# Kernel optimization log

Hardware: AMD Instinct MI355X
Metric: run time of the kernel (lower is better)

The kernel has to match this reference:

```python
import jax, jax.numpy as jnp
import numpy as np

NPOINT, RADIUS, NSAMPLE = 1024, 0.4, 32
BN_EPS = 1e-5


def fps(xyz, npoint):
    # xyz: [B, N, 3]. Deterministic start at index 0 (torch uses randint).
    B, N, _ = xyz.shape

    def step(carry, _):
        distance, farthest = carry  # [B,N], [B]
        centroid = jnp.take_along_axis(xyz, farthest[:, None, None], axis=1)  # [B,1,3]
        dist = jnp.sum((xyz - centroid) ** 2, -1)  # [B,N]
        distance = jnp.minimum(distance, dist)
        new_far = jnp.argmax(distance, axis=-1).astype(jnp.int32)
        return (distance, new_far), farthest

    init = (jnp.full((B, N), 1e10, xyz.dtype), jnp.zeros((B,), jnp.int32))
    _, cents = jax.lax.scan(step, init, None, length=npoint)  # [npoint, B]
    return cents.T  # [B, npoint]


def square_distance(src, dst):
    # src [B,S,3], dst [B,N,3] -> [B,S,N]
    d = -2.0 * jnp.einsum('bsc,bnc->bsn', src, dst)
    d = d + jnp.sum(src ** 2, -1)[:, :, None] + jnp.sum(dst ** 2, -1)[:, None, :]
    return jnp.clip(d, 1e-12, None)


def query_ball_point(radius, nsample, xyz, new_xyz):
    B, N, _ = xyz.shape
    S = new_xyz.shape[1]
    sqr = square_distance(new_xyz, xyz)  # [B,S,N]
    gi = jnp.where(sqr > radius ** 2, N, jnp.arange(N, dtype=jnp.int32)[None, None, :])
    gi = jnp.sort(gi, axis=-1)[:, :, :nsample]  # [B,S,K]
    first = gi[:, :, :1]
    return jnp.where(gi == N, first, gi)


def gather_points(points, idx):
    # points [B,N,C], idx [B,S,K] -> [B,S,K,C]
    B, S, K = idx.shape
    C = points.shape[-1]
    flat = jnp.take_along_axis(points, idx.reshape(B, S * K)[:, :, None], axis=1)
    return flat.reshape(B, S, K, C)


def setup_inputs() -> dict:
    key = jax.random.key(0)
    ks = jax.random.split(key, 10)
    B, N, D = 8, 4096, 64
    inp = {
        'xyz': jax.random.normal(ks[0], (B, 3, N), jnp.float32),
        'points': jax.random.normal(ks[1], (B, D, N), jnp.float32),
    }
    chans = [67, 64, 64, 128]
    for i in range(3):
        cin, cout = chans[i], chans[i + 1]
        inp[f'W{i}'] = jax.random.normal(ks[2 + i], (cout, cin), jnp.float32) * (1.0 / np.sqrt(cin))
        inp[f'b{i}'] = jnp.zeros((cout,), jnp.float32)
        inp[f'g{i}'] = jnp.ones((cout,), jnp.float32)
        inp[f'bt{i}'] = jnp.zeros((cout,), jnp.float32)
    return inp


def _forward(xyz, points, Ws, bs, gs, bts):
    xyz_t = jnp.transpose(xyz, (0, 2, 1))      # [B,N,3]
    pts_t = jnp.transpose(points, (0, 2, 1))   # [B,N,D]
    B, N, _ = xyz_t.shape

    fps_idx = fps(xyz_t, NPOINT)                              # [B,S]
    new_xyz = jnp.take_along_axis(xyz_t, fps_idx[:, :, None], axis=1)  # [B,S,3]
    idx = query_ball_point(RADIUS, NSAMPLE, xyz_t, new_xyz)   # [B,S,K]

    grouped_xyz = gather_points(xyz_t, idx)                   # [B,S,K,3]
    grouped_xyz_norm = grouped_xyz - new_xyz[:, :, None, :]
    grouped_pts = gather_points(pts_t, idx)                   # [B,S,K,D]
    new_points = jnp.concatenate([grouped_xyz_norm, grouped_pts], -1)  # [B,S,K,3+D]

    x = jnp.transpose(new_points, (0, 3, 2, 1))  # [B,C,K,S]
    for W, b, g, bt in zip(Ws, bs, gs, bts):
        x = jnp.einsum('oc,bcks->boks', W, x) + b[None, :, None, None]
        mean = jnp.mean(x, axis=(0, 2, 3), keepdims=True)
        var = jnp.var(x, axis=(0, 2, 3), keepdims=True)
        x = (x - mean) * jax.lax.rsqrt(var + BN_EPS)
        x = x * g[None, :, None, None] + bt[None, :, None, None]
        x = jax.nn.relu(x)
    out = jnp.max(x, axis=2)                      # [B,C_out,S]
    return jnp.transpose(new_xyz, (0, 2, 1)), out


def reference(xyz, points, W0, b0, g0, bt0, W1, b1, g1, bt1, W2, b2, g2, bt2):
    return _forward(xyz, points, (W0, W1, W2), (b0, b1, b2), (g0, g1, g2), (bt0, bt1, bt2))
```

## Files before the change

### kernel.cpp

```cpp
#include <hip/hip_runtime.h>
#include <cstddef>
#include <cstdint>

#define NB 8
#define NPTS 4096
#define NS 1024
#define NK 32
#define ND 64

#define DPP_IMAX(v, ctrl)                                                     \
  {                                                                           \
    int _o = __builtin_amdgcn_update_dpp(v, v, ctrl, 0xf, 0xf, false);        \
    v = (_o > v) ? _o : v;                                                    \
  }

#define DPP_U64MAX(hi, lo, ctrl)                                              \
  {                                                                           \
    unsigned _nh = (unsigned)__builtin_amdgcn_update_dpp((int)(hi), (int)(hi),\
                                                         ctrl, 0xf, 0xf, false);\
    unsigned _nl = (unsigned)__builtin_amdgcn_update_dpp((int)(lo), (int)(lo),\
                                                         ctrl, 0xf, 0xf, false);\
    bool _gt = (_nh > (hi)) || (_nh == (hi) && _nl > (lo));                   \
    hi = _gt ? _nh : (hi);                                                    \
    lo = _gt ? _nl : (lo);                                                    \
  }

#define DPP_FADD(v, ctrl)                                                     \
  {                                                                           \
    int _t = __builtin_amdgcn_update_dpp(__float_as_int(v), __float_as_int(v),\
                                         ctrl, 0xf, 0xf, false);              \
    v = v + __int_as_float(_t);                                               \
  }

__global__ __launch_bounds__(512) void fps_pgemm_kernel(
    const float* __restrict__ xyz, float* __restrict__ out_newxyz,
    float* __restrict__ ws_newxyz, const float* __restrict__ points,
    const float* __restrict__ W0, const float* __restrict__ b0g,
    float* __restrict__ P1) {
  __shared__ __align__(16) char smem[53376];
  const int t = threadIdx.x;

  if (blockIdx.x < 8) {
    float* sXYZ = (float*)smem;
    unsigned long long(*sRed)[8] =
        (unsigned long long(*)[8])(smem + 49152);
    int* sWidx = (int*)(smem + 49280);
    const int b = blockIdx.x;
    const int wave = t >> 6;
    const int lane = t & 63;
    const float* xb = xyz + (size_t)b * 3 * NPTS;

    for (int i = t; i < NPTS; i += 512) {
      sXYZ[i * 3 + 0] = xb[i];
      sXYZ[i * 3 + 1] = xb[NPTS + i];
      sXYZ[i * 3 + 2] = xb[2 * NPTS + i];
    }
    if (t == 0) sWidx[0] = 0;

    float px[8], py[8], pz[8], dist[8];
    {
      float4 a0 = ((const float4*)xb)[2 * t];
      float4 a1 = ((const float4*)xb)[2 * t + 1];
      float4 b0v = ((const float4*)(xb + NPTS))[2 * t];
      float4 b1v = ((const float4*)(xb + NPTS))[2 * t + 1];
      float4 c0 = ((const float4*)(xb + 2 * NPTS))[2 * t];
      float4 c1 = ((const float4*)(xb + 2 * NPTS))[2 * t + 1];
      px[0] = a0.x; px[1] = a0.y; px[2] = a0.z; px[3] = a0.w;
      px[4] = a1.x; px[5] = a1.y; px[6] = a1.z; px[7] = a1.w;
      py[0] = b0v.x; py[1] = b0v.y; py[2] = b0v.z; py[3] = b0v.w;
      py[4] = b1v.x; py[5] = b1v.y; py[6] = b1v.z; py[7] = b1v.w;
      pz[0] = c0.x; pz[1] = c0.y; pz[2] = c0.z; pz[3] = c0.w;
      pz[4] = c1.x; pz[5] = c1.y; pz[6] = c1.z; pz[7] = c1.w;
    }
#pragma unroll
    for (int j = 0; j < 8; ++j) dist[j] = 1e10f;

    float cx = xb[0], cy = xb[NPTS], cz = xb[2 * NPTS];

    for (int s = 0; s < NS; ++s) {
#pragma unroll
      for (int j = 0; j < 8; ++j) {
        float dx = __fadd_rn(px[j], -cx);
        float dy = __fadd_rn(py[j], -cy);
        float dz = __fadd_rn(pz[j], -cz);
        float d = __fadd_rn(__fadd_rn(__fmul_rn(dx, dx), __fmul_rn(dy, dy)),
                            __fmul_rn(dz, dz));
        dist[j] = fminf(dist[j], d);
      }
      float m = fmaxf(fmaxf(fmaxf(dist[0], dist[1]), fmaxf(dist[2], dist[3])),
                      fmaxf(fmaxf(dist[4], dist[5]), fmaxf(dist[6], dist[7])));
      int v = __float_as_int(m);
      DPP_IMAX(v, 0x111)
      DPP_IMAX(v, 0x112)
      DPP_IMAX(v, 0x114)
      DPP_IMAX(v, 0x118)
      DPP_IMAX(v, 0x142)
      DPP_IMAX(v, 0x143)
      const int wm_i = __builtin_amdgcn_readlane(v, 63);
      const float wm = __int_as_float(wm_i);
      unsigned long long claim = __ballot(m == wm);
      int firstlane = __ffsll(claim) - 1;
      if (lane == firstlane) {
        int j = 7;
#pragma unroll
        for (int jj = 6; jj >= 0; --jj)
          if (dist[jj] == wm) j = jj;
        unsigned widx = (unsigned)(t * 8 + j);
        sRed[s & 1][wave] = ((unsigned long long)(unsigned)wm_i << 32) |
                            (unsigned long long)(0xFFFFFFFFu - widx);
      }
      __syncthreads();
      unsigned long long k = sRed[s & 1][lane & 7];
      unsigned h2 = (unsigned)(k >> 32), l2 = (unsigned)k;
      DPP_U64MAX(h2, l2, 0x111)
      DPP_U64MAX(h2, l2, 0x112)
      DPP_U64MAX(h2, l2, 0x114)
      const unsigned gl = (unsigned)__builtin_amdgcn_readlane((int)l2, 7);
      const int widx = (int)(0xFFFFFFFFu - gl);
      cx = sXYZ[widx * 3 + 0];
      cy = sXYZ[widx * 3 + 1];
      cz = sXYZ[widx * 3 + 2];
      if (t == 0 && s < NS - 1) sWidx[s + 1] = widx;
    }
    __syncthreads();
    for (int s2 = t; s2 < NS; s2 += 512) {
      int w = sWidx[s2];
      float x = sXYZ[w * 3 + 0], y = sXYZ[w * 3 + 1], z = sXYZ[w * 3 + 2];
      out_newxyz[b * 3 * NS + s2] = x;
      out_newxyz[b * 3 * NS + NS + s2] = y;
      out_newxyz[b * 3 * NS + 2 * NS + s2] = z;
      ws_newxyz[((b << 10) + s2) * 3 + 0] = x;
      ws_newxyz[((b << 10) + s2) * 3 + 1] = y;
      ws_newxyz[((b << 10) + s2) * 3 + 2] = z;
    }
  } else {
    float* sP = (float*)smem;
    float* sW = (float*)(smem + 16384);
    float* sB = (float*)(smem + 33792);
    const int blk = blockIdx.x - 8;
    const int bb = blk >> 6;
    const int n0 = (blk & 63) * 64;
    const float* pb = points + (size_t)bb * ND * NPTS;
    for (int f = t; f < 4096; f += 512) {
      int c = f >> 6, n = f & 63;
      sP[f] = pb[c * NPTS + n0 + n];
    }
    for (int f = t; f < 4096; f += 512) {
      int c = f >> 6, o = f & 63;
      sW[c * 68 + o] = W0[o * 67 + 3 + c];
    }
    if (t < 64) sB[t] = b0g[t];
    __syncthreads();
    if (t < 256) {
      const int nl = (t & 15) * 4;
      const int ol = (t >> 4) * 4;
      float acc[4][4];
#pragma unroll
      for (int i = 0; i < 4; ++i)
#pragma unroll
        for (int j = 0; j < 4; ++j) acc[i][j] = 0.f;
#pragma unroll 4
      for (int c = 0; c < 64; ++c) {
        float4 xv = *(const float4*)(sP + c * 64 + nl);
        float4 wv = *(const float4*)(sW + c * 68 + ol);
        float xa[4] = {xv.x, xv.y, xv.z, xv.w};
        float wa[4] = {wv.x, wv.y, wv.z, wv.w};
#pragma unroll
        for (int i = 0; i < 4; ++i)
#pragma unroll
          for (int j = 0; j < 4; ++j) acc[i][j] += xa[i] * wa[j];
      }
#pragma unroll
      for (int i = 0; i < 4; ++i) {
        float4 v = make_float4(acc[i][0] + sB[ol + 0], acc[i][1] + sB[ol + 1],
                               acc[i][2] + sB[ol + 2], acc[i][3] + sB[ol + 3]);
        *(float4*)(P1 + ((size_t)(bb << 12) + n0 + nl + i) * 64 + ol) = v;
      }
    }
  }
}

__global__ __launch_bounds__(256) void query_gstats_kernel(
    const float* __restrict__ xyz, const float* __restrict__ ws_newxyz,
    const float* __restrict__ P1, const float* __restrict__ W0,
    int* __restrict__ idx_ws, float* __restrict__ partials) {
  const int w = threadIdx.x >> 6;
  const int lane = threadIdx.x & 63;
  const int p = blockIdx.x * 4 + w;
  const int b = p >> 10;
  __shared__ int sIdx[4][32];
  __shared__ float sWS[4][64];
  __shared__ float sWQ[4][64];
  const float* xb = xyz + (size_t)b * 3 * NPTS;
  const float cx = ws_newxyz[p * 3 + 0];
  const float cy = ws_newxyz[p * 3 + 1];
  const float cz = ws_newxyz[p * 3 + 2];
  const float ss = __fadd_rn(__fadd_rn(__fmul_rn(cx, cx), __fmul_rn(cy, cy)), __fmul_rn(cz, cz));
  const float r2 = (float)(0.4 * 0.4);
  int cnt = 0;
  for (int ci = 0; ci < 64 && cnt < 32; ++ci) {
    int n = ci * 64 + lane;
    float x = xb[n], y = xb[NPTS + n], z = xb[2 * NPTS + n];
    float dot = __fadd_rn(__fadd_rn(__fmul_rn(cx, x), __fmul_rn(cy, y)), __fmul_rn(cz, z));
    float dd = __fadd_rn(__fadd_rn(__fmul_rn(x, x), __fmul_rn(y, y)), __fmul_rn(z, z));
    float d = __fmul_rn(-2.0f, dot);
    d = __fadd_rn(d, ss);
    d = __fadd_rn(d, dd);
    d = fmaxf(d, 1e-12f);
    bool inc = (d <= r2);
    unsigned long long m = __ballot(inc);
    int slot = cnt + (int)__popcll(m & ((1ull << lane) - 1ull));
    if (inc && slot < 32) sIdx[w][slot] = n;
    cnt += (int)__popcll(m);
  }
  if (lane < 32) {
    int v;
    if (lane < cnt) v = sIdx[w][lane];
    else v = (cnt > 0) ? sIdx[w][0] : 0;
    idx_ws[p * 32 + lane] = v;
    sIdx[w][lane] = v;
  }
  const float wx = W0[lane * 67 + 0];
  const float wy = W0[lane * 67 + 1];
  const float wz = W0[lane * 67 + 2];
  float ssum = 0.f, ssq = 0.f;
  for (int r = 0; r < 32; ++r) {
    const int n = sIdx[w][r];
    float P1v = P1[((size_t)(b << 12) + n) * 64 + lane];
    float dx = __fadd_rn(xb[n], -cx);
    float dy = __fadd_rn(xb[NPTS + n], -cy);
    float dz = __fadd_rn(xb[2 * NPTS + n], -cz);
    float y = P1v + (dx * wx + dy * wy + dz * wz);
    ssum += y;
    ssq += y * y;
  }
  sWS[w][lane] = ssum;
  sWQ[w][lane] = ssq;
  __syncthreads();
  const int t = threadIdx.x;
  if (t < 64) {
    float s1 = sWS[0][t] + sWS[1][t] + sWS[2][t] + sWS[3][t];
    float s2 = sWQ[0][t] + sWQ[1][t] + sWQ[2][t] + sWQ[3][t];
    partials[(size_t)blockIdx.x * 128 + t] = s1;
    partials[(size_t)blockIdx.x * 128 + 64 + t] = s2;
  }
}

__global__ __launch_bounds__(256) void conv1_kernel(
    const float* __restrict__ xyz, const float* __restrict__ P1,
    const int* __restrict__ idx_ws, const float* __restrict__ cen_ws,
    const float* __restrict__ W0, const float* __restrict__ W1,
    const float* __restrict__ bias, const float* __restrict__ scaleA,
    const float* __restrict__ shiftA, float* __restrict__ y1,
    float* __restrict__ partials) {
  constexpr int CIN = 64, COUT = 64, WP = 68, TPS = 128;
  __shared__ __align__(16) float sW[CIN * WP];
  __shared__ __align__(16) float sX[2 * CIN * 32];
  __shared__ float sY[64 * 65];
  __shared__ int sIdx[64];
  __shared__ float sCen[2 * 4];
  __shared__ float sScale[CIN];
  __shared__ float sShift[CIN];
  __shared__ float sSum[COUT];
  __shared__ float sSq[COUT];

  const int t = threadIdx.x;
  const int wave = t >> 6, lane = t & 63;
  const int pair0 = blockIdx.x * 2;
  const int b = pair0 >> 10;

  for (int f = t; f < CIN * COUT; f += 256) {
    int o = f / CIN;
    int c = f - o * CIN;
    sW[c * WP + o] = W1[f];
  }
  if (t < CIN) { sScale[t] = scaleA[t]; sShift[t] = shiftA[t]; }
  if (t < COUT) { sSum[t] = 0.f; sSq[t] = 0.f; }
  if (t < 64) sIdx[t] = idx_ws[pair0 * 32 + t];
  if (t < 6) sCen[(t / 3) * 4 + (t % 3)] = cen_ws[pair0 * 3 + t];
  const float wx = W0[lane * 67 + 0];
  const float wy = W0[lane * 67 + 1];
  const float wz = W0[lane * 67 + 2];
  __syncthreads();
  const float* xb = xyz + (size_t)b * 3 * NPTS;
  for (int r = wave; r < 64; r += 4) {
    const int sl = r >> 5;
    const int n = sIdx[r];
    float P1v = P1[((size_t)(b << 12) + n) * 64 + lane];
    float dx = __fadd_rn(xb[n], -sCen[sl * 4 + 0]);
    float dy = __fadd_rn(xb[NPTS + n], -sCen[sl * 4 + 1]);
    float dz = __fadd_rn(xb[2 * NPTS + n], -sCen[sl * 4 + 2]);
    sY[r * 65 + lane] = P1v + (dx * wx + dy * wy + dz * wz);
  }
  __syncthreads();
  for (int f = t; f < 2 * CIN * 32; f += 256) {
    int sl = f >> 11;
    int rmd = f & 2047;
    int o = rmd >> 5, k = rmd & 31;
    float v = sY[(sl * 32 + k) * 65 + o];
    v = v * sScale[o] + sShift[o];
    sX[f] = fmaxf(v, 0.f);
  }
  __syncthreads();

  const int sl = t / TPS;
  const int tl = t - sl * TPS;
  const int k0 = (tl & 7) * 4;
  const int o0 = (tl >> 3) * 4;

  float acc[4][4];
#pragma unroll
  for (int i = 0; i < 4; ++i)
#pragma unroll
    for (int j = 0; j < 4; ++j) acc[i][j] = 0.f;

  const float* xrow = sX + sl * (CIN * 32);
#pragma unroll 4
  for (int c = 0; c < CIN; ++c) {
    float4 xv = *(const float4*)(xrow + c * 32 + k0);
    float4 wv = *(const float4*)(sW + c * WP + o0);
    float xa[4] = {xv.x, xv.y, xv.z, xv.w};
    float wa[4] = {wv.x, wv.y, wv.z, wv.w};
#pragma unroll
    for (int i = 0; i < 4; ++i)
#pragma unroll
      for (int j = 0; j < 4; ++j) acc[i][j] += wa[i] * xa[j];
  }
#pragma unroll
  for (int i = 0; i < 4; ++i) {
    float bo = bias[o0 + i];
#pragma unroll
    for (int j = 0; j < 4; ++j) acc[i][j] += bo;
  }
#pragma unroll
  for (int i = 0; i < 4; ++i) {
    float s1 = (acc[i][0] + acc[i][1]) + (acc[i][2] + acc[i][3]);
    float s2 = (acc[i][0] * acc[i][0] + acc[i][1] * acc[i][1]) +
               (acc[i][2] * acc[i][2] + acc[i][3] * acc[i][3]);
    DPP_FADD(s1, 0x111)
    DPP_FADD(s1, 0x112)
    DPP_FADD(s1, 0x114)
    DPP_FADD(s2, 0x111)
    DPP_FADD(s2, 0x112)
    DPP_FADD(s2, 0x114)
    if ((t & 7) == 7) {
      atomicAdd(&sSum[o0 + i], s1);
      atomicAdd(&sSq[o0 + i], s2);
    }
  }
#pragma unroll
  for (int i = 0; i < 4; ++i) {
    float4 v = make_float4(acc[i][0], acc[i][1], acc[i][2], acc[i][3]);
    *(float4*)(y1 + (size_t)(pair0 + sl) * COUT * 32 + (o0 + i) * 32 + k0) = v;
  }
  __syncthreads();
  if (t < COUT) {
    partials[(size_t)blockIdx.x * (COUT * 2) + t] = sSum[t];
    partials[(size_t)blockIdx.x * (COUT * 2) + COUT + t] = sSq[t];
  }
}

template <int CIN, int COUT, int SPB, int MODE>
__global__ __launch_bounds__(256) void conv_kernel(
    const float* __restrict__ xin, const float* __restrict__ W,
    const float* __restrict__ bias, const float* __restrict__ scaleA,
    const float* __restrict__ shiftA, float* __restrict__ yout,
    float* __restrict__ pmax, float* __restrict__ pmin,
    float* __restrict__ partials) {
  constexpr int WP = COUT + 4;
  constexpr int TPS = (COUT / 4) * 8;
  __shared__ __align__(16) float sW[CIN * WP];
  __shared__ __align__(16) float sX[SPB * CIN * 32];
  __shared__ float sScale[CIN];
  __shared__ float sShift[CIN];
  __shared__ float sSum[COUT];
  __shared__ float sSq[COUT];
  __shared__ float sMax[8 * COUT];
  __shared__ float sMin[8 * COUT];

  const int t = threadIdx.x;
  const int pair0 = blockIdx.x * SPB;

  for (int f = t; f < CIN * COUT; f += 256) {
    int o = f / CIN;
    int c = f - o * CIN;
    sW[c * WP + o] = W[f];
  }
  if (t < CIN) { sScale[t] = scaleA[t]; sShift[t] = shiftA[t]; }
  if (t < COUT) { sSum[t] = 0.f; sSq[t] = 0.f; }
  __syncthreads();

  for (int f = t; f < SPB * CIN * 32; f += 256) {
    int c = (f >> 5) % CIN;
    float v = xin[(size_t)pair0 * CIN * 32 + f];
    v = v * sScale[c] + sShift[c];
    sX[f] = fmaxf(v, 0.f);
  }
  __syncthreads();

  const int sl = t / TPS;
  const int tl = t - sl * TPS;
  const int k0 = (tl & 7) * 4;
  const int o0 = (tl >> 3) * 4;

  float acc[4][4];
#pragma unroll
  for (int i = 0; i < 4; ++i)
#pragma unroll
    for (int j = 0; j < 4; ++j) acc[i][j] = 0.f;

  const float* xrow = sX + sl * (CIN * 32);
#pragma unroll 4
  for (int c = 0; c < CIN; ++c) {
    float4 xv = *(const float4*)(xrow + c * 32 + k0);
    float4 wv = *(const float4*)(sW + c * WP + o0);
    float xa[4] = {xv.x, xv.y, xv.z, xv.w};
    float wa[4] = {wv.x, wv.y, wv.z, wv.w};
#pragma unroll
    for (int i = 0; i < 4; ++i)
#pragma unroll
      for (int j = 0; j < 4; ++j) acc[i][j] += wa[i] * xa[j];
  }
#pragma unroll
  for (int i = 0; i < 4; ++i) {
    float bo = bias[o0 + i];
#pragma unroll
    for (int j = 0; j < 4; ++j) acc[i][j] += bo;
  }
#pragma unroll
  for (int i = 0; i < 4; ++i) {
    float s1 = (acc[i][0] + acc[i][1]) + (acc[i][2] + acc[i][3]);
    float s2 = (acc[i][0] * acc[i][0] + acc[i][1] * acc[i][1]) +
               (acc[i][2] * acc[i][2] + acc[i][3] * acc[i][3]);
    DPP_FADD(s1, 0x111)
    DPP_FADD(s1, 0x112)
    DPP_FADD(s1, 0x114)
    DPP_FADD(s2, 0x111)
    DPP_FADD(s2, 0x112)
    DPP_FADD(s2, 0x114)
    if ((t & 7) == 7) {
      atomicAdd(&sSum[o0 + i], s1);
      atomicAdd(&sSq[o0 + i], s2);
    }
  }
  if (MODE < 2) {
#pragma unroll
    for (int i = 0; i < 4; ++i) {
      float4 v = make_float4(acc[i][0], acc[i][1], acc[i][2], acc[i][3]);
      *(float4*)(yout + (size_t)(pair0 + sl) * COUT * 32 + (o0 + i) * 32 + k0) = v;
    }
  } else {
#pragma unroll
    for (int i = 0; i < 4; ++i) {
      float mx = fmaxf(fmaxf(acc[i][0], acc[i][1]), fmaxf(acc[i][2], acc[i][3]));
      float mn = fminf(fminf(acc[i][0], acc[i][1]), fminf(acc[i][2], acc[i][3]));
      sMax[(k0 >> 2) * COUT + o0 + i] = mx;
      sMin[(k0 >> 2) * COUT + o0 + i] = mn;
    }
  }
  __syncthreads();
  if (t < COUT) {
    partials[(size_t)blockIdx.x * (COUT * 2) + t] = sSum[t];
    partials[(size_t)blockIdx.x * (COUT * 2) + COUT + t] = sSq[t];
    if (MODE == 2) {
      float mx = sMax[t];
      float mn = sMin[t];
#pragma unroll
      for (int q = 1; q < 8; ++q) {
        mx = fmaxf(mx, sMax[q * COUT + t]);
        mn = fminf(mn, sMin[q * COUT + t]);
      }
      pmax[pair0 * COUT + t] = mx;
      pmin[pair0 * COUT + t] = mn;
    }
  }
}

template <int COUT>
__global__ __launch_bounds__(256) void stats_kernel(const float* __restrict__ partials,
                                                    int nblocks,
                                                    const float* __restrict__ gA,
                                                    const float* __restrict__ btA,
                                                    float* __restrict__ scaleA,
                                                    float* __restrict__ shiftA) {
  const int o = blockIdx.x;
  const int t = threadIdx.x;
  double s1 = 0.0, s2 = 0.0;
  for (int blk = t; blk < nblocks; blk += 256) {
    s1 += (double)partials[(size_t)blk * (COUT * 2) + o];
    s2 += (double)partials[(size_t)blk * (COUT * 2) + COUT + o];
  }
  __shared__ double r1[256], r2[256];
  r1[t] = s1; r2[t] = s2;
  __syncthreads();
  for (int st = 128; st > 0; st >>= 1) {
    if (t < st) { r1[t] += r1[t + st]; r2[t] += r2[t + st]; }
    __syncthreads();
  }
  if (t == 0) {
    const double Nr = 262144.0;
    double mean = r1[0] / Nr;
    double var = r2[0] / Nr - mean * mean;
    double rstd = 1.0 / sqrt(var + 1e-5);
    double sc = rstd * (double)gA[o];
    scaleA[o] = (float)sc;
    shiftA[o] = (float)((double)btA[o] - mean * sc);
  }
}

__global__ __launch_bounds__(256) void stats_final_kernel(
    const float* __restrict__ partials, int nblocks,
    const float* __restrict__ pmax, const float* __restrict__ pmin,
    const float* __restrict__ gA, const float* __restrict__ btA,
    float* __restrict__ out) {
  const int o = blockIdx.x;
  const int t = threadIdx.x;
  double s1 = 0.0, s2 = 0.0;
  for (int blk = t; blk < nblocks; blk += 256) {
    s1 += (double)partials[(size_t)blk * 256 + o];
    s2 += (double)partials[(size_t)blk * 256 + 128 + o];
  }
  __shared__ double r1[256], r2[256];
  __shared__ float sMean, sRstd;
  r1[t] = s1; r2[t] = s2;
  __syncthreads();
  for (int st = 128; st > 0; st >>= 1) {
    if (t < st) { r1[t] += r1[t + st]; r2[t] += r2[t + st]; }
    __syncthreads();
  }
  if (t == 0) {
    const double Nr = 262144.0;
    double mean = r1[0] / Nr;
    double var = r2[0] / Nr - mean * mean;
    sMean = (float)mean;
    sRstd = (float)(1.0 / sqrt(var + 1e-5));
  }
  __syncthreads();
  const float mn = sMean, rs = sRstd, gg = gA[o], bb = btA[o];
  const float slope = rs * gg;
  const float* src = (slope >= 0.f) ? pmax : pmin;
  for (int i = t; i < NB * NS; i += 256) {
    int b = i >> 10;
    int s = i & 1023;
    float v = src[(size_t)i * 128 + o];
    float t1 = (v - mn) * rs;
    float t2 = t1 * gg + bb;
    out[(size_t)b * (128 * NS) + o * NS + s] = fmaxf(t2, 0.f);
  }
}

extern "C" void kernel_launch(void* const* d_in, const int* in_sizes, int n_in,
                              void* d_out, int out_size, void* d_ws, size_t ws_size,
                              hipStream_t stream) {
  (void)in_sizes; (void)n_in; (void)out_size; (void)ws_size;
  const float* xyz = (const float*)d_in[0];
  const float* points = (const float*)d_in[1];
  const float* W0 = (const float*)d_in[2];
  const float* b0 = (const float*)d_in[3];
  const float* g0 = (const float*)d_in[4];
  const float* bt0 = (const float*)d_in[5];
  const float* W1 = (const float*)d_in[6];
  const float* b1 = (const float*)d_in[7];
  const float* g1 = (const float*)d_in[8];
  const float* bt1 = (const float*)d_in[9];
  const float* W2 = (const float*)d_in[10];
  const float* b2 = (const float*)d_in[11];
  const float* g2 = (const float*)d_in[12];
  const float* bt2 = (const float*)d_in[13];
  float* out = (float*)d_out;

  float* ws = (float*)d_ws;
  size_t off = 0;
  float* newxyz = ws + off;  off += (size_t)NB * NS * 3;
  int* idx = (int*)(ws + off); off += (size_t)NB * NS * NK;
  float* P1 = ws + off;      off += (size_t)NB * NPTS * 64;
  float* y1 = ws + off;      off += (size_t)NB * NS * 64 * 32;
  float* partials = ws + off; off += (size_t)8192 * 256;
  float* scaleA = ws + off;  off += 128;
  float* shiftA = ws + off;  off += 128;
  float* pmaxb = ws + off;   off += (size_t)NB * NS * 128;
  float* pminb = ws + off;   off += (size_t)NB * NS * 128;

  fps_pgemm_kernel<<<520, 512, 0, stream>>>(xyz, out, newxyz, points, W0, b0, P1);
  query_gstats_kernel<<<2048, 256, 0, stream>>>(xyz, newxyz, P1, W0, idx, partials);
  stats_kernel<64><<<64, 256, 0, stream>>>(partials, 2048, g0, bt0, scaleA, shiftA);
  conv1_kernel<<<4096, 256, 0, stream>>>(xyz, P1, idx, newxyz, W0, W1, b1,
                                         scaleA, shiftA, y1, partials);
  stats_kernel<64><<<64, 256, 0, stream>>>(partials, 4096, g1, bt1, scaleA, shiftA);
  conv_kernel<64, 128, 1, 2><<<8192, 256, 0, stream>>>(
      y1, W2, b2, scaleA, shiftA, nullptr, pmaxb, pminb, partials);
  stats_final_kernel<<<128, 256, 0, stream>>>(partials, 8192, pmaxb, pminb,
                                              g2, bt2, out + NB * NS * 3);
}
```

Baseline: 1.043 ms.

## Run FPS in a single wavefront with packed float2 math, removing block barriers

The farthest-point-sampling blocks shrink from 512 threads to one 64-lane wavefront, each lane holding 64 points in registers as float2 pairs. The per-iteration cross-wave reduction through shared memory and __syncthreads is replaced by DPP max, a ballot and a shuffle, so there is no block barrier across the 1024 sequential steps. Packed float2 arithmetic targets the dual-issue FP32 path, and centroids are now written as they are found instead of in a final pass. In exchange each FPS lane does 8x more work per step, and the register footprint is large. The GEMM blocks sharing this kernel also drop to 64 threads with 8x8 tiles, which cuts their parallelism. The tie-break order (lowest index) matches the old code, but the packed arithmetic is no longer forced to the explicitly rounded __fadd_rn/__fmul_rn form, so results could differ slightly.

```diff
diff --git a/kernel.cpp b/kernel.cpp
--- a/kernel.cpp
+++ b/kernel.cpp
@@ -8,21 +8,12 @@
 #define NK 32
 #define ND 64
 
+typedef __attribute__((ext_vector_type(2))) float f32x2;
+
 #define DPP_IMAX(v, ctrl)                                                     \
   {                                                                           \
     int _o = __builtin_amdgcn_update_dpp(v, v, ctrl, 0xf, 0xf, false);        \
     v = (_o > v) ? _o : v;                                                    \
-  }
-
-#define DPP_U64MAX(hi, lo, ctrl)                                              \
-  {                                                                           \
-    unsigned _nh = (unsigned)__builtin_amdgcn_update_dpp((int)(hi), (int)(hi),\
-                                                         ctrl, 0xf, 0xf, false);\
-    unsigned _nl = (unsigned)__builtin_amdgcn_update_dpp((int)(lo), (int)(lo),\
-                                                         ctrl, 0xf, 0xf, false);\
-    bool _gt = (_nh > (hi)) || (_nh == (hi) && _nl > (lo));                   \
-    hi = _gt ? _nh : (hi);                                                    \
-    lo = _gt ? _nl : (lo);                                                    \
   }
 
 #define DPP_FADD(v, ctrl)                                                     \
@@ -32,63 +23,78 @@
     v = v + __int_as_float(_t);                                               \
   }
 
-__global__ __launch_bounds__(512) void fps_pgemm_kernel(
+__global__ __launch_bounds__(64, 1) void fps_pgemm_kernel(
     const float* __restrict__ xyz, float* __restrict__ out_newxyz,
     float* __restrict__ ws_newxyz, const float* __restrict__ points,
     const float* __restrict__ W0, const float* __restrict__ b0g,
     float* __restrict__ P1) {
-  __shared__ __align__(16) char smem[53376];
+  __shared__ __align__(16) char smem[49152];
   const int t = threadIdx.x;
 
   if (blockIdx.x < 8) {
-    float* sXYZ = (float*)smem;
-    unsigned long long(*sRed)[8] =
-        (unsigned long long(*)[8])(smem + 49152);
-    int* sWidx = (int*)(smem + 49280);
+    float* sX3 = (float*)smem;
     const int b = blockIdx.x;
-    const int wave = t >> 6;
-    const int lane = t & 63;
+    const int lane = t;
     const float* xb = xyz + (size_t)b * 3 * NPTS;
 
-    for (int i = t; i < NPTS; i += 512) {
-      sXYZ[i * 3 + 0] = xb[i];
-      sXYZ[i * 3 + 1] = xb[NPTS + i];
-      sXYZ[i * 3 + 2] = xb[2 * NPTS + i];
-    }
-    if (t == 0) sWidx[0] = 0;
-
-    float px[8], py[8], pz[8], dist[8];
-    {
-      float4 a0 = ((const float4*)xb)[2 * t];
-      float4 a1 = ((const float4*)xb)[2 * t + 1];
-      float4 b0v = ((const float4*)(xb + NPTS))[2 * t];
-      float4 b1v = ((const float4*)(xb + NPTS))[2 * t + 1];
-      float4 c0 = ((const float4*)(xb + 2 * NPTS))[2 * t];
-      float4 c1 = ((const float4*)(xb + 2 * NPTS))[2 * t + 1];
-      px[0] = a0.x; px[1] = a0.y; px[2] = a0.z; px[3] = a0.w;
-      px[4] = a1.x; px[5] = a1.y; px[6] = a1.z; px[7] = a1.w;
-      py[0] = b0v.x; py[1] = b0v.y; py[2] = b0v.z; py[3] = b0v.w;
-      py[4] = b1v.x; py[5] = b1v.y; py[6] = b1v.z; py[7] = b1v.w;
-      pz[0] = c0.x; pz[1] = c0.y; pz[2] = c0.z; pz[3] = c0.w;
-      pz[4] = c1.x; pz[5] = c1.y; pz[6] = c1.z; pz[7] = c1.w;
-    }
-#pragma unroll
-    for (int j = 0; j < 8; ++j) dist[j] = 1e10f;
+    for (int i = t; i < NPTS; i += 64) {
+      sX3[i * 3 + 0] = xb[i];
+      sX3[i * 3 + 1] = xb[NPTS + i];
+      sX3[i * 3 + 2] = xb[2 * NPTS + i];
+    }
+
+    f32x2 px[32], py[32], pz[32], dd[32];
+#pragma unroll
+    for (int q = 0; q < 16; ++q) {
+      float4 a = ((const float4*)xb)[lane * 16 + q];
+      float4 bq = ((const float4*)(xb + NPTS))[lane * 16 + q];
+      float4 c = ((const float4*)(xb + 2 * NPTS))[lane * 16 + q];
+      px[2 * q] = (f32x2){a.x, a.y};
+      px[2 * q + 1] = (f32x2){a.z, a.w};
+      py[2 * q] = (f32x2){bq.x, bq.y};
+      py[2 * q + 1] = (f32x2){bq.z, bq.w};
+      pz[2 * q] = (f32x2){c.x, c.y};
+      pz[2 * q + 1] = (f32x2){c.z, c.w};
+    }
+#pragma unroll
+    for (int j = 0; j < 32; ++j) dd[j] = (f32x2){1e10f, 1e10f};
 
     float cx = xb[0], cy = xb[NPTS], cz = xb[2 * NPTS];
 
     for (int s = 0; s < NS; ++s) {
-#pragma unroll
-      for (int j = 0; j < 8; ++j) {
-        float dx = __fadd_rn(px[j], -cx);
-        float dy = __fadd_rn(py[j], -cy);
-        float dz = __fadd_rn(pz[j], -cz);
-        float d = __fadd_rn(__fadd_rn(__fmul_rn(dx, dx), __fmul_rn(dy, dy)),
-                            __fmul_rn(dz, dz));
-        dist[j] = fminf(dist[j], d);
+      if (lane == 0) {
+        out_newxyz[b * 3 * NS + s] = cx;
+        out_newxyz[b * 3 * NS + NS + s] = cy;
+        out_newxyz[b * 3 * NS + 2 * NS + s] = cz;
+        ws_newxyz[((b << 10) + s) * 3 + 0] = cx;
+        ws_newxyz[((b << 10) + s) * 3 + 1] = cy;
+        ws_newxyz[((b << 10) + s) * 3 + 2] = cz;
       }
-      float m = fmaxf(fmaxf(fmaxf(dist[0], dist[1]), fmaxf(dist[2], dist[3])),
-                      fmaxf(fmaxf(dist[4], dist[5]), fmaxf(dist[6], dist[7])));
+      const f32x2 c2x = (f32x2){cx, cx};
+      const f32x2 c2y = (f32x2){cy, cy};
+      const f32x2 c2z = (f32x2){cz, cz};
+#pragma unroll
+      for (int j = 0; j < 32; ++j) {
+        f32x2 dx = px[j] - c2x;
+        f32x2 dy = py[j] - c2y;
+        f32x2 dz = pz[j] - c2z;
+        f32x2 d = (dx * dx + dy * dy) + dz * dz;
+        dd[j] = __builtin_elementwise_min(dd[j], d);
+      }
+      f32x2 r16[16];
+#pragma unroll
+      for (int i = 0; i < 16; ++i)
+        r16[i] = __builtin_elementwise_max(dd[2 * i], dd[2 * i + 1]);
+#pragma unroll
+      for (int i = 0; i < 8; ++i)
+        r16[i] = __builtin_elementwise_max(r16[2 * i], r16[2 * i + 1]);
+#pragma unroll
+      for (int i = 0; i < 4; ++i)
+        r16[i] = __builtin_elementwise_max(r16[2 * i], r16[2 * i + 1]);
+      f32x2 ra = __builtin_elementwise_max(r16[0], r16[1]);
+      f32x2 rb = __builtin_elementwise_max(r16[2], r16[3]);
+      f32x2 rr = __builtin_elementwise_max(ra, rb);
+      float m = fmaxf(rr.x, rr.y);
       int v = __float_as_int(m);
       DPP_IMAX(v, 0x111)
       DPP_IMAX(v, 0x112)
@@ -100,38 +106,16 @@
       const float wm = __int_as_float(wm_i);
       unsigned long long claim = __ballot(m == wm);
       int firstlane = __ffsll(claim) - 1;
-      if (lane == firstlane) {
-        int j = 7;
-#pragma unroll
-        for (int jj = 6; jj >= 0; --jj)
-          if (dist[jj] == wm) j = jj;
-        unsigned widx = (unsigned)(t * 8 + j);
-        sRed[s & 1][wave] = ((unsigned long long)(unsigned)wm_i << 32) |
-                            (unsigned long long)(0xFFFFFFFFu - widx);
+      int j = 63;
+#pragma unroll
+      for (int jj = 31; jj >= 0; --jj) {
+        if (dd[jj].y == wm) j = 2 * jj + 1;
+        if (dd[jj].x == wm) j = 2 * jj;
       }
-      __syncthreads();
-      unsigned long long k = sRed[s & 1][lane & 7];
-      unsigned h2 = (unsigned)(k >> 32), l2 = (unsigned)k;
-      DPP_U64MAX(h2, l2, 0x111)
-      DPP_U64MAX(h2, l2, 0x112)
-      DPP_U64MAX(h2, l2, 0x114)
-      const unsigned gl = (unsigned)__builtin_amdgcn_readlane((int)l2, 7);
-      const int widx = (int)(0xFFFFFFFFu - gl);
-      cx = sXYZ[widx * 3 + 0];
-      cy = sXYZ[widx * 3 + 1];
-      cz = sXYZ[widx * 3 + 2];
-      if (t == 0 && s < NS - 1) sWidx[s + 1] = widx;
-    }
-    __syncthreads();
-    for (int s2 = t; s2 < NS; s2 += 512) {
-      int w = sWidx[s2];
-      float x = sXYZ[w * 3 + 0], y = sXYZ[w * 3 + 1], z = sXYZ[w * 3 + 2];
-      out_newxyz[b * 3 * NS + s2] = x;
-      out_newxyz[b * 3 * NS + NS + s2] = y;
-      out_newxyz[b * 3 * NS + 2 * NS + s2] = z;
-      ws_newxyz[((b << 10) + s2) * 3 + 0] = x;
-      ws_newxyz[((b << 10) + s2) * 3 + 1] = y;
-      ws_newxyz[((b << 10) + s2) * 3 + 2] = z;
+      const int widx = __shfl(lane * 64 + j, firstlane);
+      cx = sX3[widx * 3 + 0];
+      cy = sX3[widx * 3 + 1];
+      cz = sX3[widx * 3 + 2];
     }
   } else {
     float* sP = (float*)smem;
@@ -141,41 +125,44 @@
     const int bb = blk >> 6;
     const int n0 = (blk & 63) * 64;
     const float* pb = points + (size_t)bb * ND * NPTS;
-    for (int f = t; f < 4096; f += 512) {
+    for (int f = t; f < 4096; f += 64) {
       int c = f >> 6, n = f & 63;
       sP[f] = pb[c * NPTS + n0 + n];
     }
-    for (int f = t; f < 4096; f += 512) {
+    for (int f = t; f < 4096; f += 64) {
       int c = f >> 6, o = f & 63;
       sW[c * 68 + o] = W0[o * 67 + 3 + c];
     }
-    if (t < 64) sB[t] = b0g[t];
-    __syncthreads();
-    if (t < 256) {
-      const int nl = (t & 15) * 4;
-      const int ol = (t >> 4) * 4;
-      float acc[4][4];
-#pragma unroll
-      for (int i = 0; i < 4; ++i)
-#pragma unroll
-        for (int j = 0; j < 4; ++j) acc[i][j] = 0.f;
-#pragma unroll 4
-      for (int c = 0; c < 64; ++c) {
-        float4 xv = *(const float4*)(sP + c * 64 + nl);
-        float4 wv = *(const float4*)(sW + c * 68 + ol);
-        float xa[4] = {xv.x, xv.y, xv.z, xv.w};
-        float wa[4] = {wv.x, wv.y, wv.z, wv.w};
-#pragma unroll
-        for (int i = 0; i < 4; ++i)
-#pragma unroll
-          for (int j = 0; j < 4; ++j) acc[i][j] += xa[i] * wa[j];
-      }
-#pragma unroll
-      for (int i = 0; i < 4; ++i) {
-        float4 v = make_float4(acc[i][0] + sB[ol + 0], acc[i][1] + sB[ol + 1],
-                               acc[i][2] + sB[ol + 2], acc[i][3] + sB[ol + 3]);
-        *(float4*)(P1 + ((size_t)(bb << 12) + n0 + nl + i) * 64 + ol) = v;
-      }
+    sB[t] = b0g[t];
+    const int nl = (t & 7) * 8;
+    const int ol = (t >> 3) * 8;
+    float acc[8][8];
+#pragma unroll
+    for (int i = 0; i < 8; ++i)
+#pragma unroll
+      for (int j = 0; j < 8; ++j) acc[i][j] = 0.f;
+#pragma unroll 2
+    for (int c = 0; c < 64; ++c) {
+      float4 x0 = *(const float4*)(sP + c * 64 + nl);
+      float4 x1 = *(const float4*)(sP + c * 64 + nl + 4);
+      float4 w0 = *(const float4*)(sW + c * 68 + ol);
+      float4 w1 = *(const float4*)(sW + c * 68 + ol + 4);
+      float xa[8] = {x0.x, x0.y, x0.z, x0.w, x1.x, x1.y, x1.z, x1.w};
+      float wa[8] = {w0.x, w0.y, w0.z, w0.w, w1.x, w1.y, w1.z, w1.w};
+#pragma unroll
+      for (int i = 0; i < 8; ++i)
+#pragma unroll
+        for (int j = 0; j < 8; ++j) acc[i][j] += xa[i] * wa[j];
+    }
+#pragma unroll
+    for (int i = 0; i < 8; ++i) {
+      float4 v0 = make_float4(acc[i][0] + sB[ol + 0], acc[i][1] + sB[ol + 1],
+                              acc[i][2] + sB[ol + 2], acc[i][3] + sB[ol + 3]);
+      float4 v1 = make_float4(acc[i][4] + sB[ol + 4], acc[i][5] + sB[ol + 5],
+                              acc[i][6] + sB[ol + 6], acc[i][7] + sB[ol + 7]);
+      float* dst = P1 + ((size_t)(bb << 12) + n0 + nl + i) * 64 + ol;
+      *(float4*)dst = v0;
+      *(float4*)(dst + 4) = v1;
     }
   }
 }
@@ -581,7 +568,7 @@
   float* pmaxb = ws + off;   off += (size_t)NB * NS * 128;
   float* pminb = ws + off;   off += (size_t)NB * NS * 128;
 
-  fps_pgemm_kernel<<<520, 512, 0, stream>>>(xyz, out, newxyz, points, W0, b0, P1);
+  fps_pgemm_kernel<<<520, 64, 0, stream>>>(xyz, out, newxyz, points, W0, b0, P1);
   query_gstats_kernel<<<2048, 256, 0, stream>>>(xyz, newxyz, P1, W0, idx, partials);
   stats_kernel<64><<<64, 256, 0, stream>>>(partials, 2048, g0, bt0, scaleA, shiftA);
   conv1_kernel<<<4096, 256, 0, stream>>>(xyz, P1, idx, newxyz, W0, W1, b1,
```

New measurement: 1.759 ms. +68.6%, slower.

## Replace final conv layer with bf16 MFMA kernel and DPP row reductions

Applied to the files above, without the earlier changes.

Swaps the scalar-FMA third conv layer for a kernel using 16x16x32 bf16 MFMA instructions. Weights and the normalized, ReLU'd activations are converted to bf16 in LDS with padded rows. Per-channel sum, sum of squares, max and min are computed with 16-lane DPP reductions, which replaces shared-memory atomics. The change is meant to cut FP32 ALU cost on the largest GEMM, but it loses precision from bf16 rounding of the inputs, which feed the batch statistics and the max output, and it still reloads and converts W2 in every block.

```diff
diff --git a/kernel.cpp b/kernel.cpp
--- a/kernel.cpp
+++ b/kernel.cpp
@@ -7,6 +7,15 @@
 #define NS 1024
 #define NK 32
 #define ND 64
+
+typedef __attribute__((ext_vector_type(8))) short bf16x8;
+typedef __attribute__((ext_vector_type(4))) float f32x4;
+
+__device__ __forceinline__ short f2bf(float f) {
+  unsigned u = __float_as_uint(f);
+  u += 0x7FFF + ((u >> 16) & 1);
+  return (short)(u >> 16);
+}
 
 #define DPP_IMAX(v, ctrl)                                                     \
   {                                                                           \
@@ -31,6 +40,21 @@
                                          ctrl, 0xf, 0xf, false);              \
     v = v + __int_as_float(_t);                                               \
   }
+
+#define DPP_RED16(v, OP)                                                      \
+  {                                                                           \
+    int _i;                                                                   \
+    _i = __builtin_amdgcn_update_dpp(__float_as_int(v), __float_as_int(v), 0x111, 0xf, 0xf, false); \
+    v = OP(v, __int_as_float(_i));                                            \
+    _i = __builtin_amdgcn_update_dpp(__float_as_int(v), __float_as_int(v), 0x112, 0xf, 0xf, false); \
+    v = OP(v, __int_as_float(_i));                                            \
+    _i = __builtin_amdgcn_update_dpp(__float_as_int(v), __float_as_int(v), 0x114, 0xf, 0xf, false); \
+    v = OP(v, __int_as_float(_i));                                            \
+    _i = __builtin_amdgcn_update_dpp(__float_as_int(v), __float_as_int(v), 0x118, 0xf, 0xf, false); \
+    v = OP(v, __int_as_float(_i));                                            \
+  }
+
+__device__ __forceinline__ float fadd_op(float a, float b) { return a + b; }
 
 __global__ __launch_bounds__(512) void fps_pgemm_kernel(
     const float* __restrict__ xyz, float* __restrict__ out_newxyz,
@@ -360,119 +384,86 @@
   }
 }
 
-template <int CIN, int COUT, int SPB, int MODE>
-__global__ __launch_bounds__(256) void conv_kernel(
-    const float* __restrict__ xin, const float* __restrict__ W,
-    const float* __restrict__ bias, const float* __restrict__ scaleA,
-    const float* __restrict__ shiftA, float* __restrict__ yout,
-    float* __restrict__ pmax, float* __restrict__ pmin,
-    float* __restrict__ partials) {
-  constexpr int WP = COUT + 4;
-  constexpr int TPS = (COUT / 4) * 8;
-  __shared__ __align__(16) float sW[CIN * WP];
-  __shared__ __align__(16) float sX[SPB * CIN * 32];
-  __shared__ float sScale[CIN];
-  __shared__ float sShift[CIN];
-  __shared__ float sSum[COUT];
-  __shared__ float sSq[COUT];
-  __shared__ float sMax[8 * COUT];
-  __shared__ float sMin[8 * COUT];
+__global__ __launch_bounds__(256) void conv2_mfma_kernel(
+    const float* __restrict__ y1, const float* __restrict__ W2,
+    const float* __restrict__ b2, const float* __restrict__ scaleA,
+    const float* __restrict__ shiftA, float* __restrict__ pmax,
+    float* __restrict__ pmin, float* __restrict__ partials) {
+  __shared__ __align__(16) short sW2[128 * 72];
+  __shared__ __align__(16) short sXb[32 * 72];
+  __shared__ float sScale[64], sShift[64], sBias[128];
+  __shared__ float sSum[128], sSq[128], sMax[128], sMin[128];
 
   const int t = threadIdx.x;
-  const int pair0 = blockIdx.x * SPB;
-
-  for (int f = t; f < CIN * COUT; f += 256) {
-    int o = f / CIN;
-    int c = f - o * CIN;
-    sW[c * WP + o] = W[f];
-  }
-  if (t < CIN) { sScale[t] = scaleA[t]; sShift[t] = shiftA[t]; }
-  if (t < COUT) { sSum[t] = 0.f; sSq[t] = 0.f; }
-  __syncthreads();
-
-  for (int f = t; f < SPB * CIN * 32; f += 256) {
-    int c = (f >> 5) % CIN;
-    float v = xin[(size_t)pair0 * CIN * 32 + f];
-    v = v * sScale[c] + sShift[c];
-    sX[f] = fmaxf(v, 0.f);
-  }
-  __syncthreads();
-
-  const int sl = t / TPS;
-  const int tl = t - sl * TPS;
-  const int k0 = (tl & 7) * 4;
-  const int o0 = (tl >> 3) * 4;
-
-  float acc[4][4];
-#pragma unroll
-  for (int i = 0; i < 4; ++i)
-#pragma unroll
-    for (int j = 0; j < 4; ++j) acc[i][j] = 0.f;
-
-  const float* xrow = sX + sl * (CIN * 32);
-#pragma unroll 4
-  for (int c = 0; c < CIN; ++c) {
-    float4 xv = *(const float4*)(xrow + c * 32 + k0);
-    float4 wv = *(const float4*)(sW + c * WP + o0);
-    float xa[4] = {xv.x, xv.y, xv.z, xv.w};
-    float wa[4] = {wv.x, wv.y, wv.z, wv.w};
-#pragma unroll
-    for (int i = 0; i < 4; ++i)
-#pragma unroll
-      for (int j = 0; j < 4; ++j) acc[i][j] += wa[i] * xa[j];
-  }
-#pragma unroll
-  for (int i = 0; i < 4; ++i) {
-    float bo = bias[o0 + i];
-#pragma unroll
-    for (int j = 0; j < 4; ++j) acc[i][j] += bo;
-  }
-#pragma unroll
-  for (int i = 0; i < 4; ++i) {
-    float s1 = (acc[i][0] + acc[i][1]) + (acc[i][2] + acc[i][3]);
-    float s2 = (acc[i][0] * acc[i][0] + acc[i][1] * acc[i][1]) +
-               (acc[i][2] * acc[i][2] + acc[i][3] * acc[i][3]);
-    DPP_FADD(s1, 0x111)
-    DPP_FADD(s1, 0x112)
-    DPP_FADD(s1, 0x114)
-    DPP_FADD(s2, 0x111)
-    DPP_FADD(s2, 0x112)
-    DPP_FADD(s2, 0x114)
-    if ((t & 7) == 7) {
-      atomicAdd(&sSum[o0 + i], s1);
-      atomicAdd(&sSq[o0 + i], s2);
-    }
-  }
-  if (MODE < 2) {
-#pragma unroll
-    for (int i = 0; i < 4; ++i) {
-      float4 v = make_float4(acc[i][0], acc[i][1], acc[i][2], acc[i][3]);
-      *(float4*)(yout + (size_t)(pair0 + sl) * COUT * 32 + (o0 + i) * 32 + k0) = v;
-    }
-  } else {
-#pragma unroll
-    for (int i = 0; i < 4; ++i) {
-      float mx = fmaxf(fmaxf(acc[i][0], acc[i][1]), fmaxf(acc[i][2], acc[i][3]));
-      float mn = fminf(fminf(acc[i][0], acc[i][1]), fminf(acc[i][2], acc[i][3]));
-      sMax[(k0 >> 2) * COUT + o0 + i] = mx;
-      sMin[(k0 >> 2) * COUT + o0 + i] = mn;
-    }
-  }
-  __syncthreads();
-  if (t < COUT) {
-    partials[(size_t)blockIdx.x * (COUT * 2) + t] = sSum[t];
-    partials[(size_t)blockIdx.x * (COUT * 2) + COUT + t] = sSq[t];
-    if (MODE == 2) {
-      float mx = sMax[t];
-      float mn = sMin[t];
-#pragma unroll
-      for (int q = 1; q < 8; ++q) {
-        mx = fmaxf(mx, sMax[q * COUT + t]);
-        mn = fminf(mn, sMin[q * COUT + t]);
+  const int s = blockIdx.x;
+  const int lane = t & 63;
+  const int wv = t >> 6;
+  const int quad = lane >> 4;
+  const int l15 = lane & 15;
+
+  if (t < 64) { sScale[t] = scaleA[t]; sShift[t] = shiftA[t]; }
+  if (t < 128) sBias[t] = b2[t];
+  for (int f = t; f < 8192; f += 256) {
+    int o = f >> 6, c = f & 63;
+    sW2[o * 72 + c] = f2bf(W2[f]);
+  }
+  for (int f = t; f < 2048; f += 256) {
+    int o = f >> 5, k = f & 31;
+    float v = y1[(size_t)s * 2048 + f];
+    v = v * sScale[o] + sShift[o];
+    v = fmaxf(v, 0.f);
+    sXb[k * 72 + o] = f2bf(v);
+  }
+  __syncthreads();
+
+  f32x4 a00 = {0.f, 0.f, 0.f, 0.f}, a01 = {0.f, 0.f, 0.f, 0.f};
+  f32x4 a10 = {0.f, 0.f, 0.f, 0.f}, a11 = {0.f, 0.f, 0.f, 0.f};
+#pragma unroll
+  for (int kh = 0; kh < 2; ++kh) {
+    const int kc = kh * 32 + quad * 8;
+    bf16x8 A0 = *(const bf16x8*)(sW2 + (wv * 32 + l15) * 72 + kc);
+    bf16x8 A1 = *(const bf16x8*)(sW2 + (wv * 32 + 16 + l15) * 72 + kc);
+    bf16x8 B0 = *(const bf16x8*)(sXb + l15 * 72 + kc);
+    bf16x8 B1 = *(const bf16x8*)(sXb + (16 + l15) * 72 + kc);
+    a00 = __builtin_amdgcn_mfma_f32_16x16x32_bf16(A0, B0, a00, 0, 0, 0);
+    a01 = __builtin_amdgcn_mfma_f32_16x16x32_bf16(A0, B1, a01, 0, 0, 0);
+    a10 = __builtin_amdgcn_mfma_f32_16x16x32_bf16(A1, B0, a10, 0, 0, 0);
+    a11 = __builtin_amdgcn_mfma_f32_16x16x32_bf16(A1, B1, a11, 0, 0, 0);
+  }
+
+#pragma unroll
+  for (int mi = 0; mi < 2; ++mi) {
+    f32x4 L = mi ? a10 : a00;
+    f32x4 R = mi ? a11 : a01;
+    const int m0 = wv * 32 + mi * 16;
+#pragma unroll
+    for (int reg = 0; reg < 4; ++reg) {
+      const int m = m0 + quad * 4 + reg;
+      const float bb = sBias[m];
+      float v0 = L[reg] + bb;
+      float v1 = R[reg] + bb;
+      float s1 = v0 + v1;
+      float s2 = v0 * v0 + v1 * v1;
+      float mx = fmaxf(v0, v1);
+      float mn = fminf(v0, v1);
+      DPP_RED16(s1, fadd_op)
+      DPP_RED16(s2, fadd_op)
+      DPP_RED16(mx, fmaxf)
+      DPP_RED16(mn, fminf)
+      if (l15 == 15) {
+        sSum[m] = s1;
+        sSq[m] = s2;
+        sMax[m] = mx;
+        sMin[m] = mn;
       }
-      pmax[pair0 * COUT + t] = mx;
-      pmin[pair0 * COUT + t] = mn;
-    }
+    }
+  }
+  __syncthreads();
+  if (t < 128) {
+    partials[(size_t)s * 256 + t] = sSum[t];
+    partials[(size_t)s * 256 + 128 + t] = sSq[t];
+    pmax[(size_t)s * 128 + t] = sMax[t];
+    pmin[(size_t)s * 128 + t] = sMin[t];
   }
 }
 
@@ -587,8 +578,8 @@
   conv1_kernel<<<4096, 256, 0, stream>>>(xyz, P1, idx, newxyz, W0, W1, b1,
                                          scaleA, shiftA, y1, partials);
   stats_kernel<64><<<64, 256, 0, stream>>>(partials, 4096, g1, bt1, scaleA, shiftA);
-  conv_kernel<64, 128, 1, 2><<<8192, 256, 0, stream>>>(
-      y1, W2, b2, scaleA, shiftA, nullptr, pmaxb, pminb, partials);
+  conv2_mfma_kernel<<<8192, 256, 0, stream>>>(y1, W2, b2, scaleA, shiftA,
+                                              pmaxb, pminb, partials);
   stats_final_kernel<<<128, 256, 0, stream>>>(partials, 8192, pmaxb, pminb,
                                               g2, bt2, out + NB * NS * 3);
 }
```

Measured after the change: 1.009 ms. 1.03x faster.
